# Performance work log

Hardware: AMD Instinct MI355X
Metric: run time of the kernel (lower is better)

## Reference

```python
import jax, jax.numpy as jnp
import numpy as np

N, E, G = 100000, 3200000, 256
IN_C, HID = 3, 32


def setup_inputs() -> dict:
    key = jax.random.key(0)
    ks = jax.random.split(key, 10)
    x = jax.random.normal(ks[0], (N, IN_C), dtype=jnp.float32)
    edge_index = jax.random.randint(ks[1], (2, E), 0, N, dtype=jnp.int64)
    edge_weight = jax.random.uniform(ks[2], (E,), dtype=jnp.float32)
    batch = jnp.sort(jax.random.randint(ks[3], (N,), 0, G, dtype=jnp.int64))
    # GCNConv params (PyG: out = norm-agg(x @ W) + b), glorot-ish init
    W0 = jax.random.normal(ks[4], (IN_C, HID), dtype=jnp.float32) / np.sqrt(IN_C)
    b0 = jnp.zeros((HID,), dtype=jnp.float32)
    W1 = jax.random.normal(ks[5], (HID, HID), dtype=jnp.float32) / np.sqrt(HID)
    b1 = jnp.zeros((HID,), dtype=jnp.float32)
    Wr = jax.random.normal(ks[6], (HID, 1), dtype=jnp.float32) / np.sqrt(HID)
    br = jnp.zeros((1,), dtype=jnp.float32)
    return {"x": x, "edge_index": edge_index, "edge_weight": edge_weight,
            "batch": batch, "W0": W0, "b0": b0, "W1": W1, "b1": b1,
            "Wr": Wr, "br": br}


def _gcn_conv(x, row, col, w_edge, W, b, n_nodes):
    # PyG GCNConv with add_self_loops + symmetric normalization
    h = x @ W                                   # [N, H]
    deg = jax.ops.segment_sum(w_edge, col, num_segments=n_nodes)
    dinv = jnp.where(deg > 0, jax.lax.rsqrt(deg), 0.0)
    norm = dinv[row] * w_edge * dinv[col]       # [E+N]
    msg = h[row] * norm[:, None]                # gather + scale
    agg = jax.ops.segment_sum(msg, col, num_segments=n_nodes)
    return agg + b


def reference(x, edge_index, edge_weight, batch, W0, b0, W1, b1, Wr, br):
    n = x.shape[0]
    loop = jnp.arange(n, dtype=edge_index.dtype)
    row = jnp.concatenate([edge_index[0], loop])   # source (j)
    col = jnp.concatenate([edge_index[1], loop])   # target (i)
    w = jnp.concatenate([edge_weight, jnp.ones((n,), dtype=edge_weight.dtype)])

    h = jax.nn.relu(_gcn_conv(x, row, col, w, W0, b0, n))
    h = jax.nn.relu(_gcn_conv(h, row, col, w, W1, b1, n))

    # global_mean_pool over graphs
    ones = jnp.ones((n,), dtype=h.dtype)
    cnt = jax.ops.segment_sum(ones, batch, num_segments=G)
    summed = jax.ops.segment_sum(h, batch, num_segments=G)
    hg = summed / jnp.maximum(cnt, 1.0)[:, None]   # [G, H]
    return (hg @ Wr + br).squeeze(-1)              # [G]
```

## Files before the change

kernel.cpp:

```cpp
#include <hip/hip_runtime.h>
#include <hip/hip_fp16.h>


#define TPB 256
#define NBMAX 512
#define BSH 8
#define BSZ 256
#define CAP 9216
#define ST 512
#define SV 16
#define STILE (ST * SV)

typedef unsigned long long u64;
union H8 { float4 f4; __half2 h2[4]; };
union H4 { u64 u; __half2 h2[2]; };
union HU { __half h; unsigned short u; };

__global__ void k_init(unsigned* cursor, float* gsum, float* gcnt, int nb, int g) {
    int t = threadIdx.x;
    for (int j = t; j < nb; j += blockDim.x) cursor[j] = 0u;
    for (int j = t; j < g; j += blockDim.x) { gsum[j] = 0.0f; gcnt[j] = 0.0f; }
}

__global__ void __launch_bounds__(ST) k_scat(const int* __restrict__ row,
                       const int* __restrict__ col, const float* __restrict__ w,
                       unsigned* cursor, int2* __restrict__ tmp, int nb, int e) {
    __shared__ unsigned cl[NBMAX];
    __shared__ unsigned bl[NBMAX];
    int t = threadIdx.x;
    for (int j = t; j < nb; j += ST) cl[j] = 0u;
    __syncthreads();
    const int4* c4 = (const int4*)col;
    int e4 = e >> 2;
    int base4 = blockIdx.x * (STILE >> 2);
    int4 cv[SV / 4];
    unsigned rk[SV];
    bool vld[SV / 4];
    #pragma unroll
    for (int v = 0; v < SV / 4; ++v) {
        int i4 = base4 + t + v * ST;
        vld[v] = (i4 < e4);
        if (vld[v]) {
            cv[v] = c4[i4];
            rk[4 * v + 0] = atomicAdd(&cl[cv[v].x >> BSH], 1u);
            rk[4 * v + 1] = atomicAdd(&cl[cv[v].y >> BSH], 1u);
            rk[4 * v + 2] = atomicAdd(&cl[cv[v].z >> BSH], 1u);
            rk[4 * v + 3] = atomicAdd(&cl[cv[v].w >> BSH], 1u);
        }
    }
    int tailc = -1; unsigned tailrk = 0; int taili = 0;
    if (blockIdx.x == 0) {
        int i = (e4 << 2) + t;
        if (i < e) { taili = i; tailc = col[i]; tailrk = atomicAdd(&cl[tailc >> BSH], 1u); }
    }
    __syncthreads();
    for (int j = t; j < nb; j += ST) {
        unsigned c = cl[j];
        bl[j] = c ? atomicAdd(&cursor[j], c) : 0u;
    }
    __syncthreads();
    const int4* r4 = (const int4*)row;
    const float4* w4 = (const float4*)w;
    #pragma unroll
    for (int v = 0; v < SV / 4; ++v) {
        if (vld[v]) {
            int i4 = base4 + t + v * ST;
            int4 rr = r4[i4];
            float4 ww = w4[i4];
            int c, b; unsigned lo;
            c = cv[v].x; b = c >> BSH; lo = bl[b] + rk[4 * v + 0];
            if (lo < CAP) tmp[(size_t)b * CAP + lo] =
                make_int2((int)(((unsigned)(c & 255) << 24) | (unsigned)rr.x), __float_as_int(ww.x));
            c = cv[v].y; b = c >> BSH; lo = bl[b] + rk[4 * v + 1];
            if (lo < CAP) tmp[(size_t)b * CAP + lo] =
                make_int2((int)(((unsigned)(c & 255) << 24) | (unsigned)rr.y), __float_as_int(ww.y));
            c = cv[v].z; b = c >> BSH; lo = bl[b] + rk[4 * v + 2];
            if (lo < CAP) tmp[(size_t)b * CAP + lo] =
                make_int2((int)(((unsigned)(c & 255) << 24) | (unsigned)rr.z), __float_as_int(ww.z));
            c = cv[v].w; b = c >> BSH; lo = bl[b] + rk[4 * v + 3];
            if (lo < CAP) tmp[(size_t)b * CAP + lo] =
                make_int2((int)(((unsigned)(c & 255) << 24) | (unsigned)rr.w), __float_as_int(ww.w));
        }
    }
    if (tailc >= 0) {
        int b = tailc >> BSH; unsigned lo = bl[b] + tailrk;
        if (lo < CAP) tmp[(size_t)b * CAP + lo] =
            make_int2((int)(((unsigned)(tailc & 255) << 24) | (unsigned)row[taili]),
                      __float_as_int(w[taili]));
    }
}

__global__ void __launch_bounds__(1024) k_conv(const int2* __restrict__ tmp,
                       const unsigned* __restrict__ cursor, unsigned* __restrict__ nodeinfo,
                       float* __restrict__ dinv, unsigned* __restrict__ arr, int n) {
    __shared__ u64 pk[BSZ];
    __shared__ unsigned cur[BSZ];
    int t = threadIdx.x, b = blockIdx.x;
    if (t < BSZ) pk[t] = (u64)(1u << 24);
    __syncthreads();
    unsigned cb = cursor[b]; if (cb > CAP) cb = CAP;
    size_t base = (size_t)b * CAP;
    for (unsigned k = t; k < cb; k += 1024) {
        int2 p = tmp[base + k];
        unsigned c = (unsigned)p.x >> 24;
        u64 add = (1ull << 48) |
                  (u64)(unsigned)__float2uint_rn(__int_as_float(p.y) * 16777216.0f);
        atomicAdd(&pk[c], add);
    }
    __syncthreads();
    unsigned v = 0;
    float dwv = 1.0f;
    if (t < BSZ) {
        u64 p = pk[t];
        v = (unsigned)(p >> 48);
        dwv = (float)(p & 0xFFFFFFFFFFFFull) * (1.0f / 16777216.0f);
        cur[t] = v;
    }
    __syncthreads();
    for (int off = 1; off < BSZ; off <<= 1) {
        unsigned u = (t < BSZ && t >= off) ? cur[t - off] : 0u;
        __syncthreads();
        if (t < BSZ) cur[t] += u;
        __syncthreads();
    }
    if (t < BSZ) {
        unsigned excl = cur[t] - v;
        int node = (b << BSH) + t;
        if (node < n) {
            unsigned cc = v > 1023u ? 1023u : v;
            nodeinfo[node] = (cc << 22) | (unsigned)(base + excl);
            dinv[node] = rsqrtf(dwv);
        }
        cur[t] = excl;
    }
    __syncthreads();
    for (unsigned k = t; k < cb; k += 1024) {
        int2 p = tmp[base + k];
        unsigned c = (unsigned)p.x >> 24;
        unsigned slot = atomicAdd(&cur[c], 1u);
        HU wu; wu.h = __float2half(__int_as_float(p.y));
        arr[base + slot] = ((unsigned)(wu.u & 0x7FFFu) << 17) | ((unsigned)p.x & 0x1FFFFu);
    }
}

__global__ void k_xw0(const float* __restrict__ x, const float* __restrict__ W0,
                      const float* __restrict__ dinv, float4* __restrict__ hw4, int n) {
    int t = blockIdx.x * blockDim.x + threadIdx.x;
    if (t >= n * 4) return;
    int i = t >> 2, q = t & 3;
    float x0 = x[i * 3 + 0], x1 = x[i * 3 + 1], x2 = x[i * 3 + 2];
    float di = dinv[i];
    int cb = q * 8;
    H8 u;
    #pragma unroll
    for (int j = 0; j < 4; ++j) {
        int c = cb + 2 * j;
        float a = di * (x0 * W0[c]     + x1 * W0[32 + c]     + x2 * W0[64 + c]);
        float b = di * (x0 * W0[c + 1] + x1 * W0[32 + c + 1] + x2 * W0[64 + c + 1]);
        u.h2[j] = __float22half2_rn(make_float2(a, b));
    }
    hw4[t] = u.f4;
}

#define EDGE_ACC(V) { \
    unsigned rr = (V) & 0x1FFFFu; \
    HU wu; wu.u = (unsigned short)((V) >> 17); \
    float wv = __half2float(wu.h); \
    H4 g; g.u = hw8[(rr << 3) + q]; \
    float2 f0 = __half22float2(g.h2[0]); \
    float2 f1 = __half22float2(g.h2[1]); \
    a0.x = fmaf(wv, f0.x, a0.x); a0.y = fmaf(wv, f0.y, a0.y); \
    a1.x = fmaf(wv, f1.x, a1.x); a1.y = fmaf(wv, f1.y, a1.y); }

__global__ void __launch_bounds__(256) k_agg1(const u64* __restrict__ hw8,
                      const unsigned* __restrict__ arr, const unsigned* __restrict__ nodeinfo,
                      const float* __restrict__ dinv, const float* __restrict__ W1,
                      const float* __restrict__ b0, u64* __restrict__ out8, int n) {
    __shared__ float W1s[1024];
    __shared__ float hl[32][33];
    int tid = threadIdx.x;
    for (int j = tid; j < 1024; j += 256) W1s[j] = W1[j];
    int t = blockIdx.x * 256 + tid;
    int i = t >> 3, q = t & 7;
    if (i >= n) i = n - 1;
    int li = tid >> 3;
    unsigned info = nodeinfo[i];
    unsigned k = info & 0x3FFFFFu;
    unsigned hi = k + (info >> 22);
    int idx = (i << 3) + q;
    H4 s; s.u = hw8[idx];
    float2 a0 = __half22float2(s.h2[0]);
    float2 a1 = __half22float2(s.h2[1]);
    for (; k + 8 <= hi; k += 8) {
        unsigned v0 = __builtin_nontemporal_load(arr + k + 0);
        unsigned v1 = __builtin_nontemporal_load(arr + k + 1);
        unsigned v2 = __builtin_nontemporal_load(arr + k + 2);
        unsigned v3 = __builtin_nontemporal_load(arr + k + 3);
        unsigned v4 = __builtin_nontemporal_load(arr + k + 4);
        unsigned v5 = __builtin_nontemporal_load(arr + k + 5);
        unsigned v6 = __builtin_nontemporal_load(arr + k + 6);
        unsigned v7 = __builtin_nontemporal_load(arr + k + 7);
        EDGE_ACC(v0) EDGE_ACC(v1) EDGE_ACC(v2) EDGE_ACC(v3)
        EDGE_ACC(v4) EDGE_ACC(v5) EDGE_ACC(v6) EDGE_ACC(v7)
    }
    for (; k < hi; ++k) {
        unsigned v = __builtin_nontemporal_load(arr + k);
        EDGE_ACC(v)
    }
    float di = dinv[i];
    int cb = q << 2;
    hl[li][cb + 0] = fmaxf(di * a0.x + b0[cb + 0], 0.0f);
    hl[li][cb + 1] = fmaxf(di * a0.y + b0[cb + 1], 0.0f);
    hl[li][cb + 2] = fmaxf(di * a1.x + b0[cb + 2], 0.0f);
    hl[li][cb + 3] = fmaxf(di * a1.y + b0[cb + 3], 0.0f);
    __syncthreads();
    float o0 = 0.0f, o1 = 0.0f, o2 = 0.0f, o3 = 0.0f;
    #pragma unroll
    for (int kk = 0; kk < 32; ++kk) {
        float hv = hl[li][kk];
        const float* wr = &W1s[(kk << 5) + cb];
        o0 = fmaf(hv, wr[0], o0);
        o1 = fmaf(hv, wr[1], o1);
        o2 = fmaf(hv, wr[2], o2);
        o3 = fmaf(hv, wr[3], o3);
    }
    H4 oh;
    oh.h2[0] = __float22half2_rn(make_float2(di * o0, di * o1));
    oh.h2[1] = __float22half2_rn(make_float2(di * o2, di * o3));
    out8[idx] = oh.u;
}

__global__ void __launch_bounds__(256) k_agg2(const u64* __restrict__ hw8,
                      const unsigned* __restrict__ arr, const unsigned* __restrict__ nodeinfo,
                      const float* __restrict__ dinv, const float* __restrict__ b1,
                      const float* __restrict__ Wr, float* __restrict__ sout, int n) {
    int t = blockIdx.x * 256 + threadIdx.x;
    int i = t >> 3, q = t & 7;
    bool active = (i < n);
    int ii = active ? i : (n - 1);
    unsigned info = nodeinfo[ii];
    unsigned k = info & 0x3FFFFFu;
    unsigned hi = k + (info >> 22);
    int idx = (ii << 3) + q;
    H4 s; s.u = hw8[idx];
    float2 a0 = __half22float2(s.h2[0]);
    float2 a1 = __half22float2(s.h2[1]);
    for (; k + 8 <= hi; k += 8) {
        unsigned v0 = __builtin_nontemporal_load(arr + k + 0);
        unsigned v1 = __builtin_nontemporal_load(arr + k + 1);
        unsigned v2 = __builtin_nontemporal_load(arr + k + 2);
        unsigned v3 = __builtin_nontemporal_load(arr + k + 3);
        unsigned v4 = __builtin_nontemporal_load(arr + k + 4);
        unsigned v5 = __builtin_nontemporal_load(arr + k + 5);
        unsigned v6 = __builtin_nontemporal_load(arr + k + 6);
        unsigned v7 = __builtin_nontemporal_load(arr + k + 7);
        EDGE_ACC(v0) EDGE_ACC(v1) EDGE_ACC(v2) EDGE_ACC(v3)
        EDGE_ACC(v4) EDGE_ACC(v5) EDGE_ACC(v6) EDGE_ACC(v7)
    }
    for (; k < hi; ++k) {
        unsigned v = __builtin_nontemporal_load(arr + k);
        EDGE_ACC(v)
    }
    float di = dinv[ii];
    int cb = q << 2;
    float sp = 0.0f;
    sp = fmaf(fmaxf(di * a0.x + b1[cb + 0], 0.0f), Wr[cb + 0], sp);
    sp = fmaf(fmaxf(di * a0.y + b1[cb + 1], 0.0f), Wr[cb + 1], sp);
    sp = fmaf(fmaxf(di * a1.x + b1[cb + 2], 0.0f), Wr[cb + 2], sp);
    sp = fmaf(fmaxf(di * a1.y + b1[cb + 3], 0.0f), Wr[cb + 3], sp);
    sp += __shfl_xor(sp, 1);
    sp += __shfl_xor(sp, 2);
    sp += __shfl_xor(sp, 4);
    if (active && q == 0) sout[i] = sp;
}

__global__ void k_pool2(const float* __restrict__ sarr, const int* __restrict__ batch,
                        float* gsum, float* gcnt, int n) {
    int i = blockIdx.x * blockDim.x + threadIdx.x;
    float sp = 0.0f;
    int b = -1;
    if (i < n) { sp = sarr[i]; b = batch[i]; }
    int b0v = __shfl(b, 0, 64);
    bool uniform = (b0v >= 0) && (__ballot(b == b0v) == 0xFFFFFFFFFFFFFFFFULL);
    if (uniform) {
        #pragma unroll
        for (int off = 32; off > 0; off >>= 1) sp += __shfl_down(sp, off, 64);
        if ((threadIdx.x & 63) == 0) {
            atomicAdd(&gsum[b0v], sp);
            atomicAdd(&gcnt[b0v], 64.0f);
        }
    } else if (i < n) {
        atomicAdd(&gsum[b], sp);
        atomicAdd(&gcnt[b], 1.0f);
    }
}

__global__ void k_final(const float* gsum, const float* gcnt, const float* __restrict__ br,
                        float* out, int g) {
    int i = blockIdx.x * blockDim.x + threadIdx.x;
    if (i < g) out[i] = gsum[i] / fmaxf(gcnt[i], 1.0f) + br[0];
}

extern "C" void kernel_launch(void* const* d_in, const int* in_sizes, int n_in,
                              void* d_out, int out_size, void* d_ws, size_t ws_size,
                              hipStream_t stream) {
    const float* x     = (const float*)d_in[0];
    const int*   ei    = (const int*)d_in[1];
    const float* ew    = (const float*)d_in[2];
    const int*   batch = (const int*)d_in[3];
    const float* W0    = (const float*)d_in[4];
    const float* b0    = (const float*)d_in[5];
    const float* W1    = (const float*)d_in[6];
    const float* b1    = (const float*)d_in[7];
    const float* Wr    = (const float*)d_in[8];
    const float* br    = (const float*)d_in[9];
    float* out = (float*)d_out;

    int n = in_sizes[0] / 3;
    int e = in_sizes[2];
    int g = out_size;
    const int* row = ei;
    const int* col = ei + e;
    int nb = (n + BSZ - 1) >> BSH;

    char* ws = (char*)d_ws;
    size_t off = 0;
    auto alloc = [&](size_t bytes) -> void* {
        void* p = ws + off;
        off += (bytes + 255) & ~(size_t)255;
        return p;
    };
    unsigned* cursor   = (unsigned*)alloc((size_t)NBMAX * 4);
    unsigned* nodeinfo = (unsigned*)alloc((size_t)n * 4);
    float*    dinv     = (float*)   alloc((size_t)n * 4);
    float*    sout     = (float*)   alloc((size_t)n * 4);
    float*    gsum     = (float*)   alloc((size_t)g * 4);
    float*    gcnt     = (float*)   alloc((size_t)g * 4);
    unsigned* arr      = (unsigned*)alloc((size_t)nb * CAP * 4);
    char*     region   = (char*)    alloc((size_t)nb * CAP * 8);
    int2*   tmp  = (int2*)region;
    __half* hWh1 = (__half*)region;
    __half* hWh2 = (__half*)(region + (size_t)n * 64);
    (void)ws_size;

    int stiles = (e + STILE - 1) / STILE;
    int nbk    = (n + TPB - 1) / TPB;
    int nq4    = (n * 4 + TPB - 1) / TPB;
    int nq8    = (n * 8 + TPB - 1) / TPB;

    k_init  <<<1,      1024, 0, stream>>>(cursor, gsum, gcnt, nb, g);
    k_scat  <<<stiles, ST,   0, stream>>>(row, col, ew, cursor, tmp, nb, e);
    k_conv  <<<nb,     1024, 0, stream>>>(tmp, cursor, nodeinfo, dinv, arr, n);
    k_xw0   <<<nq4,    TPB,  0, stream>>>(x, W0, dinv, (float4*)hWh1, n);
    k_agg1  <<<nq8,    TPB,  0, stream>>>((const u64*)hWh1, arr, nodeinfo, dinv, W1, b0, (u64*)hWh2, n);
    k_agg2  <<<nq8,    TPB,  0, stream>>>((const u64*)hWh2, arr, nodeinfo, dinv, b1, Wr, sout, n);
    k_pool2 <<<nbk,    TPB,  0, stream>>>(sout, batch, gsum, gcnt, n);
    k_final <<<1,      TPB,  0, stream>>>(gsum, gcnt, br, out, g);
}
```

Before: 281.0 us.

## Stage scattered edge records in shared memory for coalesced global writes

The scatter kernel now runs a block-wide prefix sum over bucket counts, places each edge record into a shared-memory staging buffer sorted by bucket, and then writes contiguous runs to global memory. The per-block tile is halved so the staging buffer fits in LDS. The conversion kernel likewise builds the sorted node array in shared memory and writes it out linearly. The aim is to replace scattered global stores with coalesced ones, at the cost of more LDS use, extra barriers, and lower occupancy.

```diff
diff --git a/kernel.cpp b/kernel.cpp
--- a/kernel.cpp
+++ b/kernel.cpp
@@ -8,7 +8,7 @@
 #define BSZ 256
 #define CAP 9216
 #define ST 512
-#define SV 16
+#define SV 8
 #define STILE (ST * SV)
 
 typedef unsigned long long u64;
@@ -27,8 +27,12 @@
                        unsigned* cursor, int2* __restrict__ tmp, int nb, int e) {
     __shared__ unsigned cl[NBMAX];
     __shared__ unsigned bl[NBMAX];
+    __shared__ unsigned lofs[NBMAX];
+    __shared__ unsigned tot_s;
+    __shared__ int2 stage[STILE];
+    __shared__ unsigned short bid[STILE];
     int t = threadIdx.x;
-    for (int j = t; j < nb; j += ST) cl[j] = 0u;
+    for (int j = t; j < NBMAX; j += ST) cl[j] = 0u;
     __syncthreads();
     const int4* c4 = (const int4*)col;
     int e4 = e >> 2;
@@ -54,10 +58,20 @@
         if (i < e) { taili = i; tailc = col[i]; tailrk = atomicAdd(&cl[tailc >> BSH], 1u); }
     }
     __syncthreads();
-    for (int j = t; j < nb; j += ST) {
-        unsigned c = cl[j];
-        bl[j] = c ? atomicAdd(&cursor[j], c) : 0u;
-    }
+    unsigned v0 = cl[t];
+    lofs[t] = v0;
+    __syncthreads();
+    for (int off = 1; off < NBMAX; off <<= 1) {
+        unsigned u = (t >= off) ? lofs[t - off] : 0u;
+        __syncthreads();
+        lofs[t] += u;
+        __syncthreads();
+    }
+    unsigned incl = lofs[t];
+    if (t == NBMAX - 1) tot_s = incl;
+    __syncthreads();
+    lofs[t] = incl - v0;
+    bl[t] = (t < nb && v0) ? atomicAdd(&cursor[t], v0) : 0u;
     __syncthreads();
     const int4* r4 = (const int4*)row;
     const float4* w4 = (const float4*)w;
@@ -67,19 +81,19 @@
             int i4 = base4 + t + v * ST;
             int4 rr = r4[i4];
             float4 ww = w4[i4];
-            int c, b; unsigned lo;
-            c = cv[v].x; b = c >> BSH; lo = bl[b] + rk[4 * v + 0];
-            if (lo < CAP) tmp[(size_t)b * CAP + lo] =
-                make_int2((int)(((unsigned)(c & 255) << 24) | (unsigned)rr.x), __float_as_int(ww.x));
-            c = cv[v].y; b = c >> BSH; lo = bl[b] + rk[4 * v + 1];
-            if (lo < CAP) tmp[(size_t)b * CAP + lo] =
-                make_int2((int)(((unsigned)(c & 255) << 24) | (unsigned)rr.y), __float_as_int(ww.y));
-            c = cv[v].z; b = c >> BSH; lo = bl[b] + rk[4 * v + 2];
-            if (lo < CAP) tmp[(size_t)b * CAP + lo] =
-                make_int2((int)(((unsigned)(c & 255) << 24) | (unsigned)rr.z), __float_as_int(ww.z));
-            c = cv[v].w; b = c >> BSH; lo = bl[b] + rk[4 * v + 3];
-            if (lo < CAP) tmp[(size_t)b * CAP + lo] =
-                make_int2((int)(((unsigned)(c & 255) << 24) | (unsigned)rr.w), __float_as_int(ww.w));
+            int c, b; unsigned li;
+            c = cv[v].x; b = c >> BSH; li = lofs[b] + rk[4 * v + 0];
+            stage[li] = make_int2((int)(((unsigned)(c & 255) << 24) | (unsigned)rr.x), __float_as_int(ww.x));
+            bid[li] = (unsigned short)b;
+            c = cv[v].y; b = c >> BSH; li = lofs[b] + rk[4 * v + 1];
+            stage[li] = make_int2((int)(((unsigned)(c & 255) << 24) | (unsigned)rr.y), __float_as_int(ww.y));
+            bid[li] = (unsigned short)b;
+            c = cv[v].z; b = c >> BSH; li = lofs[b] + rk[4 * v + 2];
+            stage[li] = make_int2((int)(((unsigned)(c & 255) << 24) | (unsigned)rr.z), __float_as_int(ww.z));
+            bid[li] = (unsigned short)b;
+            c = cv[v].w; b = c >> BSH; li = lofs[b] + rk[4 * v + 3];
+            stage[li] = make_int2((int)(((unsigned)(c & 255) << 24) | (unsigned)rr.w), __float_as_int(ww.w));
+            bid[li] = (unsigned short)b;
         }
     }
     if (tailc >= 0) {
@@ -88,6 +102,14 @@
             make_int2((int)(((unsigned)(tailc & 255) << 24) | (unsigned)row[taili]),
                       __float_as_int(w[taili]));
     }
+    __syncthreads();
+    unsigned tot = tot_s;
+    for (unsigned j = t; j < tot; j += ST) {
+        int2 rec = stage[j];
+        unsigned b = bid[j];
+        unsigned lo = bl[b] + (j - lofs[b]);
+        if (lo < CAP) tmp[(size_t)b * CAP + lo] = rec;
+    }
 }
 
 __global__ void __launch_bounds__(1024) k_conv(const int2* __restrict__ tmp,
@@ -95,6 +117,7 @@
                        float* __restrict__ dinv, unsigned* __restrict__ arr, int n) {
     __shared__ u64 pk[BSZ];
     __shared__ unsigned cur[BSZ];
+    __shared__ unsigned srec[CAP];
     int t = threadIdx.x, b = blockIdx.x;
     if (t < BSZ) pk[t] = (u64)(1u << 24);
     __syncthreads();
@@ -139,8 +162,11 @@
         unsigned c = (unsigned)p.x >> 24;
         unsigned slot = atomicAdd(&cur[c], 1u);
         HU wu; wu.h = __float2half(__int_as_float(p.y));
-        arr[base + slot] = ((unsigned)(wu.u & 0x7FFFu) << 17) | ((unsigned)p.x & 0x1FFFFu);
-    }
+        srec[slot] = ((unsigned)(wu.u & 0x7FFFu) << 17) | ((unsigned)p.x & 0x1FFFFu);
+    }
+    __syncthreads();
+    for (unsigned k = t; k < cb; k += 1024)
+        arr[base + k] = srec[k];
 }
 
 __global__ void k_xw0(const float* __restrict__ x, const float* __restrict__ W0,
```

Result: faster. 265.4 us (-5.6%).
